# Kernel optimization log

Measured on AMD Instinct MI355X. Metric: run time of the kernel, lower is better.

The kernel has to match this reference:

```python
import jax, jax.numpy as jnp
import numpy as np

LAMBDA_ENTROPY = 0.1
LAMBDA_REPULSION = 0.5
LAMBDA_INTER = 0.3
TEMPERATURE = 1.0
EPS = 1e-8


def setup_inputs() -> dict:
    key = jax.random.key(0)
    k1, k2 = jax.random.split(key)
    membership = jax.random.uniform(k1, (16384, 64, 32), dtype=jnp.float32)   # (N,F,K) soft bin assignments
    teacher_preds = jax.random.uniform(k2, (16384, 128), dtype=jnp.float32)   # (N,C)
    return {"membership": membership, "teacher_preds": teacher_preds}


def reference(membership, teacher_preds):
    N, F, K = membership.shape
    # --- weighted centroids per (feature, bin) ---
    bin_mass = membership.sum(axis=0) + EPS                       # (F,K)
    sum_weighted_y = jnp.einsum('nfk,nc->fkc', membership, teacher_preds)  # avoids (N,F,K,C)
    centroids = sum_weighted_y / bin_mass[..., None]              # (F,K,C)
    # --- weighted intra-bin variance: ||y_n - c_fk||^2 expanded, no (N,F,K,C) tensor ---
    y_sq = jnp.sum(teacher_preds * teacher_preds, axis=-1)        # (N,)
    c_sq = jnp.sum(centroids * centroids, axis=-1)                # (F,K)
    cross = jnp.einsum('nc,fkc->nfk', teacher_preds, centroids)   # (N,F,K)
    dist_sq = y_sq[:, None, None] + c_sq[None, :, :] - 2.0 * cross
    weighted_variance = jnp.sum(membership * dist_sq, axis=0) / bin_mass  # (F,K)
    loss_dispersion = weighted_variance.sum()
    # --- bin-occupancy entropy ---
    p_bins = bin_mass / N                                         # (F,K)
    loss_entropy = jnp.sum(p_bins * jnp.log(p_bins + EPS))
    # --- neighbor repulsion between adjacent bin centroids ---
    neighbor_dist = jnp.sum((centroids[:, :-1, :] - centroids[:, 1:, :]) ** 2, axis=-1)  # (F,K-1)
    loss_repulsion = jnp.sum(jnp.exp(-neighbor_dist / TEMPERATURE))
    # --- all-pairs inter-bin dispersion, batched over F (replaces python loop) ---
    dots = jnp.einsum('fkc,fjc->fkj', centroids, centroids)       # (F,K,K)
    pairwise = c_sq[:, :, None] + c_sq[:, None, :] - 2.0 * dots
    triu = jnp.triu(jnp.ones((K, K), dtype=centroids.dtype), k=1)  # strictly upper
    loss_inter = jnp.sum(jnp.exp(-pairwise / TEMPERATURE) * triu) / F
    total = (loss_dispersion
             + LAMBDA_ENTROPY * loss_entropy
             + LAMBDA_REPULSION * loss_repulsion
             + LAMBDA_INTER * loss_inter)
    return total, loss_dispersion, loss_entropy, loss_repulsion, loss_inter
```

## Files before the change

kernel.cpp:

```cpp
#include <hip/hip_runtime.h>
#include <math.h>

#define N_PTS   16384
#define F_DIM   64
#define K_BINS  32
#define C_DIM   128
#define FK      2048
#define NB32    (N_PTS / 32)
#define CW      132
#define EPS_F   1e-8f

typedef _Float16 f16x8 __attribute__((ext_vector_type(8)));
typedef float    f32x4 __attribute__((ext_vector_type(4)));

__global__ __launch_bounds__(256) void build_ybf_k(const float* __restrict__ Y,
                                                   _Float16* __restrict__ Ybf) {
    __shared__ __align__(16) float Yl[64][132];
    __shared__ float ysql[64];
    const int t  = threadIdx.x;
    const int n0 = blockIdx.x * 64;
    const int nl = t >> 5;
    const int c4 = t & 31;
#pragma unroll
    for (int p = 0; p < 8; ++p) {
        const int n = p * 8 + nl;
        const float4 v = reinterpret_cast<const float4*>(Y + (size_t)(n0 + n) * C_DIM)[c4];
        reinterpret_cast<float4*>(Yl[n])[c4] = v;
        float sq = v.x * v.x + v.y * v.y + v.z * v.z + v.w * v.w;
#pragma unroll
        for (int m = 16; m >= 1; m >>= 1) sq += __shfl_xor(sq, m, 64);
        if (c4 == 0) ysql[n] = sq;
    }
    __syncthreads();
    for (int p = 0; p < 5; ++p) {
        const int s = t + p * 256;
        if (s < 1152) {
            const int nb2  = s / 576;
            const int r    = s % 576;
            const int ct   = r >> 6;
            const int l    = r & 63;
            const int quad = l >> 4, cl = l & 15;
            const int nloc = nb2 * 32 + quad * 8;
            f16x8 v;
            if (ct < 8) {
                const int c = ct * 16 + cl;
#pragma unroll
                for (int j = 0; j < 8; ++j) v[j] = (_Float16)Yl[nloc + j][c];
            } else if (cl == 0) {
#pragma unroll
                for (int j = 0; j < 8; ++j) v[j] = (_Float16)ysql[nloc + j];
            } else if (cl == 1) {
#pragma unroll
                for (int j = 0; j < 8; ++j) v[j] = (_Float16)1.0f;
            } else {
#pragma unroll
                for (int j = 0; j < 8; ++j) v[j] = (_Float16)0.0f;
            }
            const int nb = blockIdx.x * 2 + nb2;
            *reinterpret_cast<f16x8*>(Ybf + ((size_t)(ct * NB32 + nb) * 64 + l) * 8) = v;
        }
    }
}

__global__ __launch_bounds__(256) void gemm_k(const float* __restrict__ M,
                                              const _Float16* __restrict__ Ybf,
                                              float* __restrict__ wpart,
                                              int cn) {
    __shared__ __align__(16) _Float16 Bb[2][9][512];
    const int t    = threadIdx.x;
    const int fk0  = blockIdx.x * 64;
    const int ch   = blockIdx.y;
    const int n0   = ch * cn;
    const int nb0  = n0 >> 5;
    const int w    = t >> 6;
    const int l    = t & 63;
    const int quad = l >> 4;
    const int cl   = l & 15;
    const int fkA  = fk0 + w * 16 + cl;
    const float* mp = M + fkA;
    const int steps = cn >> 5;

    f32x4 acc[9] = {};
    float a0r[8], a1r[8];

#define STAGE(s, par)                                                          \
    {                                                                          \
        const int nb_ = nb0 + (s);                                             \
        _Pragma("unroll")                                                      \
        for (int ct = w; ct < 9; ct += 4) {                                    \
            const _Float16* g_ = Ybf + ((size_t)(ct * NB32 + nb_) * 64 + l) * 8; \
            __builtin_amdgcn_global_load_lds(                                  \
                (const __attribute__((address_space(1))) unsigned*)g_,         \
                (__attribute__((address_space(3))) unsigned*)&Bb[par][ct][0],  \
                16, 0, 0);                                                     \
        }                                                                      \
    }
#define LOADA(ar, s)                                                           \
    {                                                                          \
        const size_t nbase_ = (size_t)(n0 + (s) * 32 + quad * 8);              \
        _Pragma("unroll")                                                      \
        for (int j = 0; j < 8; ++j) ar[j] = mp[(nbase_ + j) * FK];             \
    }

    STAGE(0, 0); LOADA(a0r, 0);
    STAGE(1, 1); LOADA(a1r, 1);

    for (int s = 0; s < steps; s += 2) {
        __syncthreads();
        {
            f16x8 bf[9];
#pragma unroll
            for (int ct = 0; ct < 9; ++ct)
                bf[ct] = *reinterpret_cast<const f16x8*>(&Bb[0][ct][l * 8]);
            f16x8 af;
#pragma unroll
            for (int j = 0; j < 8; ++j) af[j] = (_Float16)a0r[j];
            __syncthreads();
            if (s + 2 < steps) { STAGE(s + 2, 0); LOADA(a0r, s + 2); }
#pragma unroll
            for (int ct = 0; ct < 9; ++ct)
                acc[ct] = __builtin_amdgcn_mfma_f32_16x16x32_f16(af, bf[ct], acc[ct], 0, 0, 0);
        }
        __syncthreads();
        {
            f16x8 bf[9];
#pragma unroll
            for (int ct = 0; ct < 9; ++ct)
                bf[ct] = *reinterpret_cast<const f16x8*>(&Bb[1][ct][l * 8]);
            f16x8 af;
#pragma unroll
            for (int j = 0; j < 8; ++j) af[j] = (_Float16)a1r[j];
            __syncthreads();
            if (s + 3 < steps) { STAGE(s + 3, 1); LOADA(a1r, s + 3); }
#pragma unroll
            for (int ct = 0; ct < 9; ++ct)
                acc[ct] = __builtin_amdgcn_mfma_f32_16x16x32_f16(af, bf[ct], acc[ct], 0, 0, 0);
        }
    }
#undef STAGE
#undef LOADA

    float* wp = wpart + (size_t)ch * FK * CW;
#pragma unroll
    for (int ct = 0; ct < 9; ++ct) {
        const int c = ct * 16 + cl;
        if (c < CW) {
#pragma unroll
            for (int r = 0; r < 4; ++r) {
                const int fk = fk0 + w * 16 + quad * 4 + r;
                wp[(size_t)fk * CW + c] = acc[ct][r];
            }
        }
    }
}

__global__ __launch_bounds__(128) void reduce_w_k(const float* __restrict__ wpart,
                                                  float* __restrict__ W, int nchunk) {
    const int idx = blockIdx.x * 128 + threadIdx.x;
    const float4* src = reinterpret_cast<const float4*>(wpart);
    const size_t cs = (size_t)FK * CW / 4;
    float4 s0 = make_float4(0.f, 0.f, 0.f, 0.f), s1 = s0, s2 = s0, s3 = s0;
    int ch = 0;
    for (; ch + 3 < nchunk; ch += 4) {
        const float4 a = src[idx + (size_t)(ch + 0) * cs];
        const float4 b = src[idx + (size_t)(ch + 1) * cs];
        const float4 c = src[idx + (size_t)(ch + 2) * cs];
        const float4 d = src[idx + (size_t)(ch + 3) * cs];
        s0.x += a.x; s0.y += a.y; s0.z += a.z; s0.w += a.w;
        s1.x += b.x; s1.y += b.y; s1.z += b.z; s1.w += b.w;
        s2.x += c.x; s2.y += c.y; s2.z += c.z; s2.w += c.w;
        s3.x += d.x; s3.y += d.y; s3.z += d.z; s3.w += d.w;
    }
    for (; ch < nchunk; ++ch) {
        const float4 a = src[idx + (size_t)ch * cs];
        s0.x += a.x; s0.y += a.y; s0.z += a.z; s0.w += a.w;
    }
    float4 r;
    r.x = (s0.x + s1.x) + (s2.x + s3.x);
    r.y = (s0.y + s1.y) + (s2.y + s3.y);
    r.z = (s0.z + s1.z) + (s2.z + s3.z);
    r.w = (s0.w + s1.w) + (s2.w + s3.w);
    reinterpret_cast<float4*>(W)[idx] = r;
}

__global__ __launch_bounds__(256) void epilogue_k(const float* __restrict__ W,
                                                  float* __restrict__ fpart) {
    __shared__ __align__(16) float Wl[32][CW];
    __shared__ float Bv[32], Binv[32], S1v[32], csq[32];
    __shared__ float scr[32][8];
    __shared__ float4 red4[256];
    const int t = threadIdx.x;
    const int f = blockIdx.x;

    for (int e = t; e < 32 * 33; e += 256) {
        const int k = e / 33, c4 = e % 33;
        reinterpret_cast<float4*>(Wl[k])[c4] =
            reinterpret_cast<const float4*>(W + (size_t)(f * 32 + k) * CW)[c4];
    }
    __syncthreads();
    if (t < 32) {
        const float B = Wl[t][129] + EPS_F;
        Bv[t] = B; Binv[t] = 1.0f / B; S1v[t] = Wl[t][128];
    }
    __syncthreads();
    {
        const int k = t >> 3, g = t & 7;
        const float ib = Binv[k];
        float s = 0.f;
        for (int c = g * 16; c < g * 16 + 16; ++c) {
            const float v = Wl[k][c] * ib;
            Wl[k][c] = v;
            s = fmaf(v, v, s);
        }
        scr[k][g] = s;
    }
    __syncthreads();
    if (t < 32) {
        float s = 0.f;
#pragma unroll
        for (int g = 0; g < 8; ++g) s += scr[t][g];
        csq[t] = s;
    }
    __syncthreads();

    float my_disp = 0.f, my_ent = 0.f, my_rep = 0.f, my_inter = 0.f;
    if (t < 32) {
        my_disp = (S1v[t] - csq[t] * (Bv[t] + EPS_F)) * Binv[t];
        const float p = Bv[t] * (1.0f / (float)N_PTS);
        my_ent = p * logf(p + EPS_F);
    }
    {
        const int pr = t >> 3, g = t & 7;
        float s = 0.f;
        if (pr < 31) {
            for (int c = g * 16; c < g * 16 + 16; ++c) {
                const float d = Wl[pr][c] - Wl[pr + 1][c];
                s = fmaf(d, d, s);
            }
        }
        __syncthreads();
        scr[pr][g] = s;
    }
    __syncthreads();
    if (t < 31) {
        float d = 0.f;
#pragma unroll
        for (int g = 0; g < 8; ++g) d += scr[t][g];
        my_rep = expf(-d);
    }
#pragma unroll
    for (int s4 = 0; s4 < 4; ++s4) {
        const int slot = t + s4 * 256;
        const int k = slot >> 5, j = slot & 31;
        if (k < j) {
            float dot = 0.f;
            for (int c4 = 0; c4 < 32; ++c4) {
                const float4 a = reinterpret_cast<const float4*>(Wl[k])[c4];
                const float4 b = reinterpret_cast<const float4*>(Wl[j])[c4];
                dot = fmaf(a.x, b.x, dot); dot = fmaf(a.y, b.y, dot);
                dot = fmaf(a.z, b.z, dot); dot = fmaf(a.w, b.w, dot);
            }
            my_inter += expf(-(csq[k] + csq[j] - 2.0f * dot));
        }
    }
    red4[t] = make_float4(my_disp, my_ent, my_rep, my_inter);
    __syncthreads();
    for (int off = 128; off >= 1; off >>= 1) {
        if (t < off) {
            const float4 a = red4[t], b = red4[t + off];
            red4[t] = make_float4(a.x + b.x, a.y + b.y, a.z + b.z, a.w + b.w);
        }
        __syncthreads();
    }
    if (t == 0) {
        fpart[f * 4 + 0] = red4[0].x;
        fpart[f * 4 + 1] = red4[0].y;
        fpart[f * 4 + 2] = red4[0].z;
        fpart[f * 4 + 3] = red4[0].w;
    }
}

__global__ void final_reduce_k(const float* __restrict__ fpart,
                               float* __restrict__ out) {
    const int t = threadIdx.x;
    float4 v = reinterpret_cast<const float4*>(fpart)[t];
#pragma unroll
    for (int m = 32; m >= 1; m >>= 1) {
        v.x += __shfl_xor(v.x, m, 64);
        v.y += __shfl_xor(v.y, m, 64);
        v.z += __shfl_xor(v.z, m, 64);
        v.w += __shfl_xor(v.w, m, 64);
    }
    if (t == 0) {
        const float disp  = v.x, ent = v.y, rep = v.z;
        const float inter = v.w * (1.0f / (float)F_DIM);
        out[0] = disp + 0.1f * ent + 0.5f * rep + 0.3f * inter;
        out[1] = disp;
        out[2] = ent;
        out[3] = rep;
        out[4] = inter;
    }
}

extern "C" void kernel_launch(void* const* d_in, const int* in_sizes, int n_in,
                              void* d_out, int out_size, void* d_ws, size_t ws_size,
                              hipStream_t stream) {
    const float* M = (const float*)d_in[0];
    const float* Y = (const float*)d_in[1];
    float* out = (float*)d_out;
    char*  ws  = (char*)d_ws;

    const size_t ybfBytes = (size_t)9 * NB32 * 64 * 8 * sizeof(_Float16);
    const size_t wBytes   = (size_t)FK * CW * sizeof(float);

    _Float16* Ybf   = (_Float16*)ws;
    float*    W     = (float*)(ws + ybfBytes);
    float*    fpart = (float*)(ws + ybfBytes + wBytes);
    float*    wpart = (float*)(ws + ybfBytes + wBytes + 1024);

    const size_t used = ybfBytes + wBytes + 1024;
    int nchunk = 32;
    while (nchunk > 1 && used + (size_t)nchunk * wBytes > ws_size) nchunk >>= 1;
    const int cn = N_PTS / nchunk;

    build_ybf_k<<<dim3(N_PTS / 64), dim3(256), 0, stream>>>(Y, Ybf);
    gemm_k<<<dim3(32, nchunk), dim3(256), 0, stream>>>(M, Ybf, wpart, cn);
    reduce_w_k<<<dim3(FK * CW / 4 / 128), dim3(128), 0, stream>>>(wpart, W, nchunk);
    epilogue_k<<<dim3(F_DIM), dim3(256), 0, stream>>>(W, fpart);
    final_reduce_k<<<dim3(1), dim3(64), 0, stream>>>(fpart, out);
}
```

Before: 229.5 us.

## Split N within GEMM blocks, halve chunk partials, fold final reduce into epilogue

The GEMM block now covers 32 fk rows and splits its 1024-point N chunk between two wave groups. Each group has its own double-buffered LDS tiles, and the two partial accumulators are combined through LDS before the store. This halves the number of chunk partials to 16, which cuts the wpart write and reduce traffic, while the grid grows to 64x16 blocks. It also drops the final_reduce kernel launch by using atomics plus a last-block counter in the epilogue. The accumulators are zeroed in build_ybf_k, so the result now depends on that kernel ordering, and the atomic float adds make the sum order nondeterministic.

```diff
diff --git a/kernel.cpp b/kernel.cpp
--- a/kernel.cpp
+++ b/kernel.cpp
@@ -9,15 +9,19 @@
 #define NB32    (N_PTS / 32)
 #define CW      132
 #define EPS_F   1e-8f
+#define NCHUNK  16
+#define CN      1024
 
 typedef _Float16 f16x8 __attribute__((ext_vector_type(8)));
 typedef float    f32x4 __attribute__((ext_vector_type(4)));
 
 __global__ __launch_bounds__(256) void build_ybf_k(const float* __restrict__ Y,
-                                                   _Float16* __restrict__ Ybf) {
+                                                   _Float16* __restrict__ Ybf,
+                                                   float* __restrict__ accs) {
     __shared__ __align__(16) float Yl[64][132];
     __shared__ float ysql[64];
     const int t  = threadIdx.x;
+    if (blockIdx.x == 0 && t < 8) accs[t] = 0.0f;
     const int n0 = blockIdx.x * 64;
     const int nl = t >> 5;
     const int c4 = t & 31;
@@ -64,21 +68,21 @@
 
 __global__ __launch_bounds__(256) void gemm_k(const float* __restrict__ M,
                                               const _Float16* __restrict__ Ybf,
-                                              float* __restrict__ wpart,
-                                              int cn) {
-    __shared__ __align__(16) _Float16 Bb[2][9][512];
+                                              float* __restrict__ wpart) {
+    __shared__ __align__(16) _Float16 Bb[2][2][9][512];
     const int t    = threadIdx.x;
-    const int fk0  = blockIdx.x * 64;
+    const int fk0  = blockIdx.x * 32;
     const int ch   = blockIdx.y;
-    const int n0   = ch * cn;
-    const int nb0  = n0 >> 5;
     const int w    = t >> 6;
+    const int g    = w >> 1;
+    const int wl   = w & 1;
     const int l    = t & 63;
     const int quad = l >> 4;
     const int cl   = l & 15;
-    const int fkA  = fk0 + w * 16 + cl;
+    const int fkA  = fk0 + wl * 16 + cl;
     const float* mp = M + fkA;
-    const int steps = cn >> 5;
+    const int n0   = ch * CN + g * 512;
+    const int nb0  = n0 >> 5;
 
     f32x4 acc[9] = {};
     float a0r[8], a1r[8];
@@ -87,11 +91,11 @@
     {                                                                          \
         const int nb_ = nb0 + (s);                                             \
         _Pragma("unroll")                                                      \
-        for (int ct = w; ct < 9; ct += 4) {                                    \
+        for (int ct = wl; ct < 9; ct += 2) {                                   \
             const _Float16* g_ = Ybf + ((size_t)(ct * NB32 + nb_) * 64 + l) * 8; \
             __builtin_amdgcn_global_load_lds(                                  \
                 (const __attribute__((address_space(1))) unsigned*)g_,         \
-                (__attribute__((address_space(3))) unsigned*)&Bb[par][ct][0],  \
+                (__attribute__((address_space(3))) unsigned*)&Bb[g][par][ct][0], \
                 16, 0, 0);                                                     \
         }                                                                      \
     }
@@ -105,18 +109,18 @@
     STAGE(0, 0); LOADA(a0r, 0);
     STAGE(1, 1); LOADA(a1r, 1);
 
-    for (int s = 0; s < steps; s += 2) {
+    for (int s = 0; s < 16; s += 2) {
         __syncthreads();
         {
             f16x8 bf[9];
 #pragma unroll
             for (int ct = 0; ct < 9; ++ct)
-                bf[ct] = *reinterpret_cast<const f16x8*>(&Bb[0][ct][l * 8]);
+                bf[ct] = *reinterpret_cast<const f16x8*>(&Bb[g][0][ct][l * 8]);
             f16x8 af;
 #pragma unroll
             for (int j = 0; j < 8; ++j) af[j] = (_Float16)a0r[j];
             __syncthreads();
-            if (s + 2 < steps) { STAGE(s + 2, 0); LOADA(a0r, s + 2); }
+            if (s + 2 < 16) { STAGE(s + 2, 0); LOADA(a0r, s + 2); }
 #pragma unroll
             for (int ct = 0; ct < 9; ++ct)
                 acc[ct] = __builtin_amdgcn_mfma_f32_16x16x32_f16(af, bf[ct], acc[ct], 0, 0, 0);
@@ -126,12 +130,12 @@
             f16x8 bf[9];
 #pragma unroll
             for (int ct = 0; ct < 9; ++ct)
-                bf[ct] = *reinterpret_cast<const f16x8*>(&Bb[1][ct][l * 8]);
+                bf[ct] = *reinterpret_cast<const f16x8*>(&Bb[g][1][ct][l * 8]);
             f16x8 af;
 #pragma unroll
             for (int j = 0; j < 8; ++j) af[j] = (_Float16)a1r[j];
             __syncthreads();
-            if (s + 3 < steps) { STAGE(s + 3, 1); LOADA(a1r, s + 3); }
+            if (s + 3 < 16) { STAGE(s + 3, 1); LOADA(a1r, s + 3); }
 #pragma unroll
             for (int ct = 0; ct < 9; ++ct)
                 acc[ct] = __builtin_amdgcn_mfma_f32_16x16x32_f16(af, bf[ct], acc[ct], 0, 0, 0);
@@ -140,15 +144,27 @@
 #undef STAGE
 #undef LOADA
 
-    float* wp = wpart + (size_t)ch * FK * CW;
-#pragma unroll
-    for (int ct = 0; ct < 9; ++ct) {
-        const int c = ct * 16 + cl;
-        if (c < CW) {
-#pragma unroll
-            for (int r = 0; r < 4; ++r) {
-                const int fk = fk0 + w * 16 + quad * 4 + r;
-                wp[(size_t)fk * CW + c] = acc[ct][r];
+    float* scr = reinterpret_cast<float*>(&Bb[0][0][0][0]);
+    if (g == 1) {
+#pragma unroll
+        for (int ct = 0; ct < 9; ++ct)
+#pragma unroll
+            for (int r = 0; r < 4; ++r)
+                scr[(wl * 16 + quad * 4 + r) * 144 + ct * 16 + cl] = acc[ct][r];
+    }
+    __syncthreads();
+    if (g == 0) {
+        float* wp = wpart + (size_t)ch * FK * CW;
+#pragma unroll
+        for (int ct = 0; ct < 9; ++ct) {
+            const int c = ct * 16 + cl;
+            if (c < CW) {
+#pragma unroll
+                for (int r = 0; r < 4; ++r) {
+                    const int row = wl * 16 + quad * 4 + r;
+                    const int fk  = fk0 + row;
+                    wp[(size_t)fk * CW + c] = acc[ct][r] + scr[row * 144 + c];
+                }
             }
         }
     }
@@ -184,7 +200,8 @@
 }
 
 __global__ __launch_bounds__(256) void epilogue_k(const float* __restrict__ W,
-                                                  float* __restrict__ fpart) {
+                                                  float* __restrict__ accs,
+                                                  float* __restrict__ out) {
     __shared__ __align__(16) float Wl[32][CW];
     __shared__ float Bv[32], Binv[32], S1v[32], csq[32];
     __shared__ float scr[32][8];
@@ -273,32 +290,26 @@
         __syncthreads();
     }
     if (t == 0) {
-        fpart[f * 4 + 0] = red4[0].x;
-        fpart[f * 4 + 1] = red4[0].y;
-        fpart[f * 4 + 2] = red4[0].z;
-        fpart[f * 4 + 3] = red4[0].w;
-    }
-}
-
-__global__ void final_reduce_k(const float* __restrict__ fpart,
-                               float* __restrict__ out) {
-    const int t = threadIdx.x;
-    float4 v = reinterpret_cast<const float4*>(fpart)[t];
-#pragma unroll
-    for (int m = 32; m >= 1; m >>= 1) {
-        v.x += __shfl_xor(v.x, m, 64);
-        v.y += __shfl_xor(v.y, m, 64);
-        v.z += __shfl_xor(v.z, m, 64);
-        v.w += __shfl_xor(v.w, m, 64);
-    }
-    if (t == 0) {
-        const float disp  = v.x, ent = v.y, rep = v.z;
-        const float inter = v.w * (1.0f / (float)F_DIM);
-        out[0] = disp + 0.1f * ent + 0.5f * rep + 0.3f * inter;
-        out[1] = disp;
-        out[2] = ent;
-        out[3] = rep;
-        out[4] = inter;
+        atomicAdd(accs + 0, red4[0].x);
+        atomicAdd(accs + 1, red4[0].y);
+        atomicAdd(accs + 2, red4[0].z);
+        atomicAdd(accs + 3, red4[0].w);
+        __threadfence();
+        const unsigned prev = __hip_atomic_fetch_add(
+            reinterpret_cast<unsigned*>(accs + 4), 1u,
+            __ATOMIC_ACQ_REL, __HIP_MEMORY_SCOPE_AGENT);
+        if (prev == (unsigned)(F_DIM - 1)) {
+            const float disp = __hip_atomic_load(accs + 0, __ATOMIC_RELAXED, __HIP_MEMORY_SCOPE_AGENT);
+            const float ent  = __hip_atomic_load(accs + 1, __ATOMIC_RELAXED, __HIP_MEMORY_SCOPE_AGENT);
+            const float rep  = __hip_atomic_load(accs + 2, __ATOMIC_RELAXED, __HIP_MEMORY_SCOPE_AGENT);
+            const float inter = __hip_atomic_load(accs + 3, __ATOMIC_RELAXED, __HIP_MEMORY_SCOPE_AGENT)
+                                * (1.0f / (float)F_DIM);
+            out[0] = disp + 0.1f * ent + 0.5f * rep + 0.3f * inter;
+            out[1] = disp;
+            out[2] = ent;
+            out[3] = rep;
+            out[4] = inter;
+        }
     }
 }
 
@@ -315,17 +326,11 @@
 
     _Float16* Ybf   = (_Float16*)ws;
     float*    W     = (float*)(ws + ybfBytes);
-    float*    fpart = (float*)(ws + ybfBytes + wBytes);
+    float*    accs  = (float*)(ws + ybfBytes + wBytes);
     float*    wpart = (float*)(ws + ybfBytes + wBytes + 1024);
 
-    const size_t used = ybfBytes + wBytes + 1024;
-    int nchunk = 32;
-    while (nchunk > 1 && used + (size_t)nchunk * wBytes > ws_size) nchunk >>= 1;
-    const int cn = N_PTS / nchunk;
-
-    build_ybf_k<<<dim3(N_PTS / 64), dim3(256), 0, stream>>>(Y, Ybf);
-    gemm_k<<<dim3(32, nchunk), dim3(256), 0, stream>>>(M, Ybf, wpart, cn);
-    reduce_w_k<<<dim3(FK * CW / 4 / 128), dim3(128), 0, stream>>>(wpart, W, nchunk);
-    epilogue_k<<<dim3(F_DIM), dim3(256), 0, stream>>>(W, fpart);
-    final_reduce_k<<<dim3(1), dim3(64), 0, stream>>>(fpart, out);
-}
+    build_ybf_k<<<dim3(N_PTS / 64), dim3(256), 0, stream>>>(Y, Ybf, accs);
+    gemm_k<<<dim3(64, NCHUNK), dim3(256), 0, stream>>>(M, Ybf, wpart);
+    reduce_w_k<<<dim3(FK * CW / 4 / 128), dim3(128), 0, stream>>>(wpart, W, NCHUNK);
+    epilogue_k<<<dim3(F_DIM), dim3(256), 0, stream>>>(W, accs, out);
+}
```

Result: slower. 238.0 us (+3.7%).
